# Optimization experiments

Measured on AMD Instinct MI355X. Metric: run time of the kernel, lower is better.

## Reference

```python
import jax, jax.numpy as jnp
import numpy as np


def _silu(v):
    return v * jax.nn.sigmoid(v)


def setup_inputs() -> dict:
    key = jax.random.key(0)
    ks = jax.random.split(key, 12)
    B, N, DS = 4, 12500, 63      # batch, nodes per graph, dim_single
    E = 800000                   # total edges (avg degree 16)
    BN = B * N
    ND = DS + 1                  # node_dim = dim_single + 1 (timestep channel)
    H, ED = 128, 32              # hidden_dim, edge_dim (fixed in __init__)
    MIN = 2 * ND + ED            # m_input feature dim = 160

    def lin(k, i, o):
        return (jax.random.normal(k, (i, o)) / np.sqrt(i)).astype(jnp.float32)

    return {
        "x": jax.random.normal(ks[0], (B, N, 3), dtype=jnp.float32) * 5.0,
        "cond": jax.random.normal(ks[1], (B, N, DS), dtype=jnp.float32),
        "edge_dist": jax.random.uniform(ks[2], (E,), dtype=jnp.float32) * 15.0,
        "ew1": lin(ks[3], 1, ED), "eb1": jnp.zeros((ED,), jnp.float32),
        "ew2": lin(ks[4], ED, ED), "eb2": jnp.zeros((ED,), jnp.float32),
        "nw1": lin(ks[5], MIN, H), "nb1": jnp.zeros((H,), jnp.float32),
        "nw2": lin(ks[6], H, ND), "nb2": jnp.zeros((ND,), jnp.float32),
        "cw1": lin(ks[7], MIN, H), "cb1": jnp.zeros((H,), jnp.float32),
        "cw2": lin(ks[8], H, 1),
        "edge_index": jax.random.randint(ks[9], (2, E), 0, BN, dtype=jnp.int64 if jax.config.jax_enable_x64 else jnp.int32),
        "t": 100,
    }


def reference(x, cond, edge_dist, ew1, eb1, ew2, eb2, nw1, nb1, nw2, nb2,
              cw1, cb1, cw2, edge_index, t):
    B, N, _ = x.shape
    BN = B * N
    # append timestep scalar channel to conditioning -> node features h
    t_feat = jnp.full((B, N, 1), t, dtype=x.dtype)
    h = jnp.concatenate([cond, t_feat], axis=-1).reshape(BN, -1)   # [BN, node_dim]
    xf = x.reshape(BN, 3)

    src, dst = edge_index[0], edge_index[1]
    # edge_mlp on scalar distances -> [E, edge_dim]
    edge_attr = _silu(edge_dist[:, None] @ ew1 + eb1) @ ew2 + eb2
    # gather + concat -> [E, 2*node_dim + edge_dim]
    m_input = jnp.concatenate([h[src], h[dst], edge_attr], axis=-1)
    # node_mlp (its output h_agg is discarded by p_sample, kept for faithfulness)
    m = _silu(m_input @ nw1 + nb1) @ nw2 + nb2
    h_agg = jax.ops.segment_sum(m, dst, num_segments=BN)
    h_out = h + h_agg  # unused by p_sample's return
    del h_out
    # coord_mlp -> scalar weight per edge
    coord_weight = _silu(m_input @ cw1 + cb1) @ cw2                 # [E, 1]
    dir_vec = xf[src] - xf[dst]                                     # [E, 3]
    dir_len = jnp.maximum(jnp.linalg.norm(dir_vec, axis=-1, keepdims=True), 1e-8)
    coord_update = coord_weight * (dir_vec / dir_len)
    x_agg = jax.ops.segment_sum(coord_update, dst, num_segments=BN)
    return (xf + x_agg).reshape(B, N, 3)
```

## Files before the change

### kernel.cpp

```cpp
#include <hip/hip_runtime.h>
#include <hip/hip_bf16.h>

typedef __attribute__((ext_vector_type(8))) short bf16x8;
typedef __attribute__((ext_vector_type(4))) float f32x4;
typedef __attribute__((ext_vector_type(4), aligned(4))) float f32x4u;
typedef __attribute__((ext_vector_type(2), aligned(4))) float f32x2u;

__device__ __forceinline__ unsigned short f2bf(float f) {
    unsigned int u = __float_as_uint(f);
    unsigned int r = (u + 0x7fffu + ((u >> 16) & 1u)) >> 16;
    return (unsigned short)r;
}

__global__ void init_out_kernel(const float* __restrict__ x, float* __restrict__ out, int n) {
    int i = blockIdx.x * blockDim.x + threadIdx.x;
    if (i < n) out[i] = x[i];
}

__global__ void prep_bt_kernel(const float* __restrict__ cw1, unsigned short* __restrict__ bt) {
    int idx = blockIdx.x * 256 + threadIdx.x;
    if (idx < 160 * 128) {
        int k = idx / 128, n = idx % 128;
        bt[n * 160 + k] = f2bf(cw1[idx]);
    }
}

__device__ __forceinline__ bf16x8 load8_bf(const float* p) {
    f32x4u a = *(const f32x4u*)p;
    f32x4u b = *(const f32x4u*)(p + 4);
    bf16x8 r;
    r[0] = f2bf(a[0]); r[1] = f2bf(a[1]); r[2] = f2bf(a[2]); r[3] = f2bf(a[3]);
    r[4] = f2bf(b[0]); r[5] = f2bf(b[1]); r[6] = f2bf(b[2]); r[7] = f2bf(b[3]);
    return r;
}
__device__ __forceinline__ bf16x8 load7t_bf(const float* p, unsigned short tbf) {
    f32x4u a = *(const f32x4u*)p;
    f32x2u b = *(const f32x2u*)(p + 4);
    float c = p[6];
    bf16x8 r;
    r[0] = f2bf(a[0]); r[1] = f2bf(a[1]); r[2] = f2bf(a[2]); r[3] = f2bf(a[3]);
    r[4] = f2bf(b[0]); r[5] = f2bf(b[1]); r[6] = f2bf(c);  r[7] = (short)tbf;
    return r;
}

__global__ __launch_bounds__(256, 4) void edge_mfma_kernel(
    const float* __restrict__ x, const float* __restrict__ cond,
    const float* __restrict__ edge_dist,
    const float* __restrict__ ew1, const float* __restrict__ eb1,
    const float* __restrict__ ew2, const float* __restrict__ eb2,
    const float* __restrict__ cb1, const float* __restrict__ cw2,
    const unsigned short* __restrict__ bt,
    const int* __restrict__ edge_index, const int* __restrict__ tptr,
    float* __restrict__ out, int E)
{
    __shared__ __align__(16) unsigned short ea_lds[128][40];
    __shared__ int srcl[128];
    __shared__ int dstl[128];
    __shared__ float cw_lds[128];

    const float tval = (float)tptr[0];
    const unsigned short tbf = f2bf(tval);
    const int tid  = threadIdx.x;
    const int lane = tid & 63;
    const int wid  = tid >> 6;
    const int e0   = blockIdx.x * 128;

    if (tid < 128) {
        int e = e0 + tid; if (e >= E) e = E - 1;
        float dist = edge_dist[e];
        float s[32];
        #pragma unroll
        for (int i = 0; i < 32; ++i) {
            float v = fmaf(dist, ew1[i], eb1[i]);
            s[i] = v / (1.f + __expf(-v));
        }
        float ea[32];
        #pragma unroll
        for (int j = 0; j < 32; ++j) ea[j] = eb2[j];
        #pragma unroll
        for (int i = 0; i < 32; ++i) {
            const float* wr = &ew2[i * 32];
            #pragma unroll
            for (int j = 0; j < 32; ++j) ea[j] = fmaf(s[i], wr[j], ea[j]);
        }
        #pragma unroll
        for (int j = 0; j < 32; ++j) ea_lds[tid][j] = f2bf(ea[j]);
    } else {
        int r = tid - 128;
        int e = e0 + r; if (e >= E) e = E - 1;
        srcl[r] = edge_index[e];
        dstl[r] = edge_index[E + e];
    }
    __syncthreads();

    const int fr = lane & 15;
    const int kq = lane >> 4;

    bf16x8 afrag[5][2];
    #pragma unroll
    for (int m = 0; m < 2; ++m) {
        int row = wid * 32 + m * 16 + fr;
        int src = srcl[row];
        int dst = dstl[row];
        const float* sp = cond + (long)src * 63;
        const float* dp = cond + (long)dst * 63;
        afrag[0][m] = load8_bf(sp + 8 * kq);
        afrag[1][m] = (kq < 3) ? load8_bf(sp + 32 + 8 * kq) : load7t_bf(sp + 56, tbf);
        afrag[2][m] = load8_bf(dp + 8 * kq);
        afrag[3][m] = (kq < 3) ? load8_bf(dp + 32 + 8 * kq) : load7t_bf(dp + 56, tbf);
        afrag[4][m] = *reinterpret_cast<const bf16x8*>(&ea_lds[row][8 * kq]);
    }

    float psum[2][4] = {{0.f,0.f,0.f,0.f},{0.f,0.f,0.f,0.f}};
    #pragma unroll 1
    for (int nh = 0; nh < 2; ++nh) {
        f32x4 acc[2][4];
        #pragma unroll
        for (int m = 0; m < 2; ++m)
            #pragma unroll
            for (int n = 0; n < 4; ++n)
                acc[m][n] = (f32x4){0.f, 0.f, 0.f, 0.f};

        #pragma unroll
        for (int k0t = 0; k0t < 5; ++k0t) {
            #pragma unroll
            for (int n = 0; n < 4; ++n) {
                int col = (nh * 4 + n) * 16 + fr;
                bf16x8 b = *reinterpret_cast<const bf16x8*>(&bt[col * 160 + k0t * 32 + 8 * kq]);
                acc[0][n] = __builtin_amdgcn_mfma_f32_16x16x32_bf16(afrag[k0t][0], b, acc[0][n], 0, 0, 0);
                acc[1][n] = __builtin_amdgcn_mfma_f32_16x16x32_bf16(afrag[k0t][1], b, acc[1][n], 0, 0, 0);
            }
        }
        #pragma unroll
        for (int n = 0; n < 4; ++n) {
            int col = (nh * 4 + n) * 16 + fr;
            float b1 = cb1[col];
            float w2 = cw2[col];
            #pragma unroll
            for (int m = 0; m < 2; ++m)
                #pragma unroll
                for (int r = 0; r < 4; ++r) {
                    float h = acc[m][n][r] + b1;
                    float sil = h / (1.f + __expf(-h));
                    psum[m][r] = fmaf(sil, w2, psum[m][r]);
                }
        }
    }

    #pragma unroll
    for (int off = 1; off < 16; off <<= 1)
        #pragma unroll
        for (int m = 0; m < 2; ++m)
            #pragma unroll
            for (int r = 0; r < 4; ++r)
                psum[m][r] += __shfl_xor(psum[m][r], off, 64);
    if (fr == 0) {
        #pragma unroll
        for (int m = 0; m < 2; ++m) {
            int row0 = wid * 32 + m * 16 + kq * 4;
            #pragma unroll
            for (int r = 0; r < 4; ++r) cw_lds[row0 + r] = psum[m][r];
        }
    }
    __syncthreads();

    if (tid < 128) {
        int e = e0 + tid;
        if (e < E) {
            float coord_w = cw_lds[tid];
            int src = srcl[tid];
            int dst = dstl[tid];
            float dx = x[src * 3 + 0] - x[dst * 3 + 0];
            float dy = x[src * 3 + 1] - x[dst * 3 + 1];
            float dz = x[src * 3 + 2] - x[dst * 3 + 2];
            float len = sqrtf(fmaf(dx, dx, fmaf(dy, dy, dz * dz)));
            len = fmaxf(len, 1e-8f);
            float sc = coord_w / len;
            atomicAdd(&out[dst * 3 + 0], sc * dx);
            atomicAdd(&out[dst * 3 + 1], sc * dy);
            atomicAdd(&out[dst * 3 + 2], sc * dz);
        }
    }
}

extern "C" void kernel_launch(void* const* d_in, const int* in_sizes, int n_in,
                              void* d_out, int out_size, void* d_ws, size_t ws_size,
                              hipStream_t stream) {
    const float* x         = (const float*)d_in[0];
    const float* cond      = (const float*)d_in[1];
    const float* edge_dist = (const float*)d_in[2];
    const float* ew1       = (const float*)d_in[3];
    const float* eb1       = (const float*)d_in[4];
    const float* ew2       = (const float*)d_in[5];
    const float* eb2       = (const float*)d_in[6];
    const float* cw1       = (const float*)d_in[11];
    const float* cb1       = (const float*)d_in[12];
    const float* cw2       = (const float*)d_in[13];
    const int*   edge_index= (const int*)d_in[14];
    const int*   tptr      = (const int*)d_in[15];
    float* out = (float*)d_out;

    const int E = in_sizes[2];
    const int n_out = out_size;

    unsigned short* bt = (unsigned short*)d_ws;

    init_out_kernel<<<(n_out + 255) / 256, 256, 0, stream>>>(x, out, n_out);
    prep_bt_kernel<<<(160 * 128 + 255) / 256, 256, 0, stream>>>(cw1, bt);

    int blocks = (E + 127) / 128;
    edge_mfma_kernel<<<blocks, 256, 0, stream>>>(x, cond, edge_dist,
                                                 ew1, eb1, ew2, eb2,
                                                 cb1, cw2, bt,
                                                 edge_index, tptr, out, E);
}
```

Before: 297.4 us.

## Precompute per-node projections and fold edge MLP into coord layer weights

The first coord-MLP layer is split by linearity. The src and dst node-feature parts are computed once per node (BN×256 bf16 table via MFMA), and the edge-attr second layer is folded with cw1 into one 32×128 matrix plus a constant bias that also absorbs the timestep channel. Each edge then runs a K=32 MFMA instead of K=160 and gathers two 128-wide bf16 rows in place of raw cond rows. This removes most per-edge matmul work and the per-thread 32×32 edge MLP. The cost is an extra node pass, a ~25MB intermediate table with scattered per-element gathers, and more bf16 rounding of the intermediate sums.

```diff
diff --git a/kernel.cpp b/kernel.cpp
--- a/kernel.cpp
+++ b/kernel.cpp
@@ -11,18 +11,44 @@
     unsigned int r = (u + 0x7fffu + ((u >> 16) & 1u)) >> 16;
     return (unsigned short)r;
 }
+__device__ __forceinline__ float bf2f(unsigned short u) {
+    return __uint_as_float(((unsigned int)u) << 16);
+}
 
 __global__ void init_out_kernel(const float* __restrict__ x, float* __restrict__ out, int n) {
     int i = blockIdx.x * blockDim.x + threadIdx.x;
     if (i < n) out[i] = x[i];
 }
 
-__global__ void prep_bt_kernel(const float* __restrict__ cw1, unsigned short* __restrict__ bt) {
+__global__ void prep_bt2_kernel(const float* __restrict__ cw1, unsigned short* __restrict__ bt2) {
     int idx = blockIdx.x * 256 + threadIdx.x;
-    if (idx < 160 * 128) {
-        int k = idx / 128, n = idx % 128;
-        bt[n * 160 + k] = f2bf(cw1[idx]);
-    }
+    if (idx < 256 * 64) {
+        int n = idx >> 6, k = idx & 63;
+        float v = 0.f;
+        if (k < 63) v = (n < 128) ? cw1[k * 128 + n] : cw1[(64 + k) * 128 + (n - 128)];
+        bt2[n * 64 + k] = f2bf(v);
+    }
+}
+
+__global__ void prep_consts_kernel(const float* __restrict__ ew2, const float* __restrict__ eb2,
+                                   const float* __restrict__ cw1, const float* __restrict__ cb1,
+                                   const int* __restrict__ tptr,
+                                   unsigned short* __restrict__ bt_M, float* __restrict__ c0) {
+    int j = threadIdx.x;
+    float t = (float)tptr[0];
+    float cacc = cb1[j] + t * (cw1[63 * 128 + j] + cw1[127 * 128 + j]);
+    float m[32];
+    #pragma unroll
+    for (int p = 0; p < 32; ++p) m[p] = 0.f;
+    for (int i = 0; i < 32; ++i) {
+        float w = cw1[(128 + i) * 128 + j];
+        cacc = fmaf(eb2[i], w, cacc);
+        #pragma unroll
+        for (int p = 0; p < 32; ++p) m[p] = fmaf(ew2[p * 32 + i], w, m[p]);
+    }
+    c0[j] = cacc;
+    #pragma unroll
+    for (int p = 0; p < 32; ++p) bt_M[j * 32 + p] = f2bf(m[p]);
 }
 
 __device__ __forceinline__ bf16x8 load8_bf(const float* p) {
@@ -33,58 +59,88 @@
     r[4] = f2bf(b[0]); r[5] = f2bf(b[1]); r[6] = f2bf(b[2]); r[7] = f2bf(b[3]);
     return r;
 }
-__device__ __forceinline__ bf16x8 load7t_bf(const float* p, unsigned short tbf) {
+__device__ __forceinline__ bf16x8 load7z_bf(const float* p) {
     f32x4u a = *(const f32x4u*)p;
     f32x2u b = *(const f32x2u*)(p + 4);
     float c = p[6];
     bf16x8 r;
     r[0] = f2bf(a[0]); r[1] = f2bf(a[1]); r[2] = f2bf(a[2]); r[3] = f2bf(a[3]);
-    r[4] = f2bf(b[0]); r[5] = f2bf(b[1]); r[6] = f2bf(c);  r[7] = (short)tbf;
+    r[4] = f2bf(b[0]); r[5] = f2bf(b[1]); r[6] = f2bf(c);  r[7] = 0;
     return r;
 }
 
-__global__ __launch_bounds__(256, 4) void edge_mfma_kernel(
-    const float* __restrict__ x, const float* __restrict__ cond,
-    const float* __restrict__ edge_dist,
+__global__ __launch_bounds__(256) void prep_uv_kernel(
+    const float* __restrict__ cond, const unsigned short* __restrict__ bt2,
+    unsigned short* __restrict__ UV, int BN)
+{
+    const int tid = threadIdx.x, lane = tid & 63, wid = tid >> 6;
+    const int fr = lane & 15, kq = lane >> 4;
+    const int base = blockIdx.x * 128 + wid * 32;
+
+    bf16x8 a[2][2];
+    #pragma unroll
+    for (int m = 0; m < 2; ++m) {
+        int node = base + m * 16 + fr; if (node >= BN) node = BN - 1;
+        const float* cp = cond + (long)node * 63;
+        a[0][m] = load8_bf(cp + 8 * kq);
+        a[1][m] = (kq < 3) ? load8_bf(cp + 32 + 8 * kq) : load7z_bf(cp + 56);
+    }
+    #pragma unroll 1
+    for (int nh = 0; nh < 2; ++nh) {
+        f32x4 acc[2][8];
+        #pragma unroll
+        for (int m = 0; m < 2; ++m)
+            #pragma unroll
+            for (int n = 0; n < 8; ++n) acc[m][n] = (f32x4){0.f, 0.f, 0.f, 0.f};
+        #pragma unroll
+        for (int n = 0; n < 8; ++n) {
+            int col = (nh * 8 + n) * 16 + fr;
+            bf16x8 b0 = *reinterpret_cast<const bf16x8*>(&bt2[col * 64 + 8 * kq]);
+            bf16x8 b1 = *reinterpret_cast<const bf16x8*>(&bt2[col * 64 + 32 + 8 * kq]);
+            acc[0][n] = __builtin_amdgcn_mfma_f32_16x16x32_bf16(a[0][0], b0, acc[0][n], 0, 0, 0);
+            acc[0][n] = __builtin_amdgcn_mfma_f32_16x16x32_bf16(a[1][0], b1, acc[0][n], 0, 0, 0);
+            acc[1][n] = __builtin_amdgcn_mfma_f32_16x16x32_bf16(a[0][1], b0, acc[1][n], 0, 0, 0);
+            acc[1][n] = __builtin_amdgcn_mfma_f32_16x16x32_bf16(a[1][1], b1, acc[1][n], 0, 0, 0);
+        }
+        #pragma unroll
+        for (int m = 0; m < 2; ++m)
+            #pragma unroll
+            for (int r = 0; r < 4; ++r) {
+                int node = base + m * 16 + kq * 4 + r;
+                if (node < BN) {
+                    #pragma unroll
+                    for (int n = 0; n < 8; ++n)
+                        UV[(long)node * 256 + (nh * 8 + n) * 16 + fr] = f2bf(acc[m][n][r]);
+                }
+            }
+    }
+}
+
+__global__ __launch_bounds__(256, 4) void edge_kernel(
+    const float* __restrict__ x, const float* __restrict__ edge_dist,
     const float* __restrict__ ew1, const float* __restrict__ eb1,
-    const float* __restrict__ ew2, const float* __restrict__ eb2,
-    const float* __restrict__ cb1, const float* __restrict__ cw2,
-    const unsigned short* __restrict__ bt,
-    const int* __restrict__ edge_index, const int* __restrict__ tptr,
-    float* __restrict__ out, int E)
+    const unsigned short* __restrict__ bt_M, const float* __restrict__ c0f,
+    const float* __restrict__ cw2, const unsigned short* __restrict__ UV,
+    const int* __restrict__ edge_index, float* __restrict__ out, int E)
 {
-    __shared__ __align__(16) unsigned short ea_lds[128][40];
+    __shared__ __align__(16) unsigned short s_lds[128][40];
     __shared__ int srcl[128];
     __shared__ int dstl[128];
     __shared__ float cw_lds[128];
 
-    const float tval = (float)tptr[0];
-    const unsigned short tbf = f2bf(tval);
-    const int tid  = threadIdx.x;
-    const int lane = tid & 63;
-    const int wid  = tid >> 6;
-    const int e0   = blockIdx.x * 128;
+    const int tid = threadIdx.x, lane = tid & 63, wid = tid >> 6;
+    const int fr = lane & 15, kq = lane >> 4;
+    const int e0 = blockIdx.x * 128;
 
     if (tid < 128) {
         int e = e0 + tid; if (e >= E) e = E - 1;
         float dist = edge_dist[e];
-        float s[32];
         #pragma unroll
         for (int i = 0; i < 32; ++i) {
             float v = fmaf(dist, ew1[i], eb1[i]);
-            s[i] = v / (1.f + __expf(-v));
-        }
-        float ea[32];
-        #pragma unroll
-        for (int j = 0; j < 32; ++j) ea[j] = eb2[j];
-        #pragma unroll
-        for (int i = 0; i < 32; ++i) {
-            const float* wr = &ew2[i * 32];
-            #pragma unroll
-            for (int j = 0; j < 32; ++j) ea[j] = fmaf(s[i], wr[j], ea[j]);
-        }
-        #pragma unroll
-        for (int j = 0; j < 32; ++j) ea_lds[tid][j] = f2bf(ea[j]);
+            float s = v / (1.f + __expf(-v));
+            s_lds[tid][i] = f2bf(s);
+        }
     } else {
         int r = tid - 128;
         int e = e0 + r; if (e >= E) e = E - 1;
@@ -93,54 +149,49 @@
     }
     __syncthreads();
 
-    const int fr = lane & 15;
-    const int kq = lane >> 4;
-
-    bf16x8 afrag[5][2];
-    #pragma unroll
-    for (int m = 0; m < 2; ++m) {
-        int row = wid * 32 + m * 16 + fr;
-        int src = srcl[row];
-        int dst = dstl[row];
-        const float* sp = cond + (long)src * 63;
-        const float* dp = cond + (long)dst * 63;
-        afrag[0][m] = load8_bf(sp + 8 * kq);
-        afrag[1][m] = (kq < 3) ? load8_bf(sp + 32 + 8 * kq) : load7t_bf(sp + 56, tbf);
-        afrag[2][m] = load8_bf(dp + 8 * kq);
-        afrag[3][m] = (kq < 3) ? load8_bf(dp + 32 + 8 * kq) : load7t_bf(dp + 56, tbf);
-        afrag[4][m] = *reinterpret_cast<const bf16x8*>(&ea_lds[row][8 * kq]);
-    }
+    bf16x8 a[2];
+    #pragma unroll
+    for (int m = 0; m < 2; ++m)
+        a[m] = *reinterpret_cast<const bf16x8*>(&s_lds[wid * 32 + m * 16 + fr][8 * kq]);
+
+    int offu[2][4], offv[2][4];
+    #pragma unroll
+    for (int m = 0; m < 2; ++m)
+        #pragma unroll
+        for (int r = 0; r < 4; ++r) {
+            int row = wid * 32 + m * 16 + kq * 4 + r;
+            offu[m][r] = srcl[row] * 256;
+            offv[m][r] = dstl[row] * 256 + 128;
+        }
 
     float psum[2][4] = {{0.f,0.f,0.f,0.f},{0.f,0.f,0.f,0.f}};
     #pragma unroll 1
     for (int nh = 0; nh < 2; ++nh) {
         f32x4 acc[2][4];
         #pragma unroll
-        for (int m = 0; m < 2; ++m)
-            #pragma unroll
-            for (int n = 0; n < 4; ++n)
-                acc[m][n] = (f32x4){0.f, 0.f, 0.f, 0.f};
-
-        #pragma unroll
-        for (int k0t = 0; k0t < 5; ++k0t) {
-            #pragma unroll
-            for (int n = 0; n < 4; ++n) {
-                int col = (nh * 4 + n) * 16 + fr;
-                bf16x8 b = *reinterpret_cast<const bf16x8*>(&bt[col * 160 + k0t * 32 + 8 * kq]);
-                acc[0][n] = __builtin_amdgcn_mfma_f32_16x16x32_bf16(afrag[k0t][0], b, acc[0][n], 0, 0, 0);
-                acc[1][n] = __builtin_amdgcn_mfma_f32_16x16x32_bf16(afrag[k0t][1], b, acc[1][n], 0, 0, 0);
-            }
+        for (int n = 0; n < 4; ++n) {
+            float c = c0f[(nh * 4 + n) * 16 + fr];
+            acc[0][n] = (f32x4){c, c, c, c};
+            acc[1][n] = (f32x4){c, c, c, c};
         }
         #pragma unroll
         for (int n = 0; n < 4; ++n) {
             int col = (nh * 4 + n) * 16 + fr;
-            float b1 = cb1[col];
+            bf16x8 b = *reinterpret_cast<const bf16x8*>(&bt_M[col * 32 + 8 * kq]);
+            acc[0][n] = __builtin_amdgcn_mfma_f32_16x16x32_bf16(a[0], b, acc[0][n], 0, 0, 0);
+            acc[1][n] = __builtin_amdgcn_mfma_f32_16x16x32_bf16(a[1], b, acc[1][n], 0, 0, 0);
+        }
+        #pragma unroll
+        for (int n = 0; n < 4; ++n) {
+            int col = (nh * 4 + n) * 16 + fr;
             float w2 = cw2[col];
             #pragma unroll
             for (int m = 0; m < 2; ++m)
                 #pragma unroll
                 for (int r = 0; r < 4; ++r) {
-                    float h = acc[m][n][r] + b1;
+                    float uf = bf2f(UV[offu[m][r] + col]);
+                    float vf = bf2f(UV[offv[m][r] + col]);
+                    float h = acc[m][n][r] + uf + vf;
                     float sil = h / (1.f + __expf(-h));
                     psum[m][r] = fmaf(sil, w2, psum[m][r]);
                 }
@@ -200,17 +251,23 @@
     const int*   tptr      = (const int*)d_in[15];
     float* out = (float*)d_out;
 
-    const int E = in_sizes[2];
+    const int E  = in_sizes[2];
+    const int BN = in_sizes[1] / 63;
     const int n_out = out_size;
 
-    unsigned short* bt = (unsigned short*)d_ws;
+    char* ws = (char*)d_ws;
+    unsigned short* bt_M = (unsigned short*)(ws);
+    float*          c0   = (float*)(ws + 8192);
+    unsigned short* bt2  = (unsigned short*)(ws + 16384);
+    unsigned short* UV   = (unsigned short*)(ws + 65536);
 
     init_out_kernel<<<(n_out + 255) / 256, 256, 0, stream>>>(x, out, n_out);
-    prep_bt_kernel<<<(160 * 128 + 255) / 256, 256, 0, stream>>>(cw1, bt);
+    prep_bt2_kernel<<<64, 256, 0, stream>>>(cw1, bt2);
+    prep_consts_kernel<<<1, 128, 0, stream>>>(ew2, eb2, cw1, cb1, tptr, bt_M, c0);
+    prep_uv_kernel<<<(BN + 127) / 128, 256, 0, stream>>>(cond, bt2, UV, BN);
 
     int blocks = (E + 127) / 128;
-    edge_mfma_kernel<<<blocks, 256, 0, stream>>>(x, cond, edge_dist,
-                                                 ew1, eb1, ew2, eb2,
-                                                 cb1, cw2, bt,
-                                                 edge_index, tptr, out, E);
-}
+    edge_kernel<<<blocks, 256, 0, stream>>>(x, edge_dist, ew1, eb1,
+                                            bt_M, c0, cw2, UV,
+                                            edge_index, out, E);
+}
```

Result: faster. 271.0 us (-8.9%).
